# Optimization experiments

Hardware: AMD Instinct MI355X
Metric: run time of the kernel (lower is better)

Reference implementation:

```python
import jax, jax.numpy as jnp
import numpy as np

N_NODES = 100000
N_EDGES = 1600000
R = 8
EPS = 1e-5


def bn_eval(x, g, b, m, v):
    # BatchNorm1d in eval mode: affine with running stats
    return (x - m) * (g / jnp.sqrt(v + EPS)) + b


def rgcn_conv(x, W, root, bias, src, dst, etype):
    # PyG RGCNConv: out[i] = sum_r mean_{j in N_r(i)} x_j W_r + x_i W_root + b
    # Transform once per relation, then gather per edge (avoids [E,in,out] weight gather).
    h = jnp.einsum('ni,rio->rno', x, W)          # [R, N, O]
    msg = h[etype, src]                           # [E, O] gather
    key = dst * R + etype                         # per-(dst, relation) segment
    ones = jnp.ones(etype.shape, dtype=x.dtype)
    deg = jax.ops.segment_sum(ones, key, num_segments=N_NODES * R)
    norm = 1.0 / jnp.maximum(deg[key], 1.0)       # mean within each relation
    agg = jax.ops.segment_sum(msg * norm[:, None], dst, num_segments=N_NODES)
    return agg + x @ root + bias


def setup_inputs() -> dict:
    key = jax.random.key(0)
    ks = jax.random.split(key, 24)
    f = jnp.float32
    inp = {
        'n_id': jax.random.randint(ks[0], (N_NODES,), 0, N_NODES),
        'edge_index': jax.random.randint(ks[1], (2, N_EDGES), 0, N_NODES),
        'edge_types': jax.random.randint(ks[2], (N_EDGES,), 0, R),
        'emb': jax.random.normal(ks[3], (N_NODES, 32), f),
        'W1': jax.random.normal(ks[4], (R, 32, 64), f) * 0.1,
        'root1': jax.random.normal(ks[5], (32, 64), f) * 0.1,
        'b1': jax.random.normal(ks[6], (64,), f) * 0.1,
        'W2': jax.random.normal(ks[7], (R, 64, 64), f) * 0.1,
        'root2': jax.random.normal(ks[8], (64, 64), f) * 0.1,
        'b2': jax.random.normal(ks[9], (64,), f) * 0.1,
        'bn32_g': jax.random.uniform(ks[10], (32,), f, 0.5, 1.5),
        'bn32_b': jax.random.normal(ks[11], (32,), f) * 0.1,
        'bn32_m': jax.random.normal(ks[12], (32,), f) * 0.1,
        'bn32_v': jax.random.uniform(ks[13], (32,), f, 0.5, 1.5),
        'bn64_g': jax.random.uniform(ks[14], (64,), f, 0.5, 1.5),
        'bn64_b': jax.random.normal(ks[15], (64,), f) * 0.1,
        'bn64_m': jax.random.normal(ks[16], (64,), f) * 0.1,
        'bn64_v': jax.random.uniform(ks[17], (64,), f, 0.5, 1.5),
        'bn64b_g': jax.random.uniform(ks[18], (64,), f, 0.5, 1.5),
        'bn64b_b': jax.random.normal(ks[19], (64,), f) * 0.1,
        'bn64b_m': jax.random.normal(ks[20], (64,), f) * 0.1,
        'bn64b_v': jax.random.uniform(ks[21], (64,), f, 0.5, 1.5),
    }
    return inp


def reference(n_id, edge_index, edge_types, emb, W1, root1, b1, W2, root2, b2,
              bn32_g, bn32_b, bn32_m, bn32_v,
              bn64_g, bn64_b, bn64_m, bn64_v,
              bn64b_g, bn64b_b, bn64b_m, bn64b_v):
    src, dst = edge_index[0], edge_index[1]
    x = emb[n_id]                                  # embedding lookup
    x = bn_eval(x, bn32_g, bn32_b, bn32_m, bn32_v)
    x = jax.nn.relu(rgcn_conv(x, W1, root1, b1, src, dst, edge_types))
    x = bn_eval(x, bn64_g, bn64_b, bn64_m, bn64_v)
    # dropout is identity in eval mode
    x = rgcn_conv(x, W2, root2, b2, src, dst, edge_types)
    x = bn_eval(x, bn64b_g, bn64b_b, bn64b_m, bn64b_v)
    return x
```

## Files before the change

kernel.cpp:

```cpp
#include <hip/hip_runtime.h>

#define EPS 1e-5f
constexpr int NN  = 100000;
constexpr int NE  = 1600000;
constexpr int R   = 8;
constexpr int NBK = NN / 16;
constexpr int CAP = 512;
constexpr int CHUNK  = 2048;
constexpr int NCHUNK = (NE + CHUNK - 1) / CHUNK;
constexpr int NBIN   = 98;
constexpr int SEGS   = 9;
constexpr int BINCAP = SEGS * CHUNK;

typedef _Float16 half8 __attribute__((ext_vector_type(8)));
typedef _Float16 h2    __attribute__((ext_vector_type(2)));
typedef float f32x4 __attribute__((ext_vector_type(4)));

static __device__ inline unsigned short f2h(float f) {
    _Float16 h = (_Float16)f;
    return __builtin_bit_cast(unsigned short, h);
}

__global__ __launch_bounds__(256) void compute_x0(
    const int* __restrict__ n_id, const float* __restrict__ emb,
    const float* __restrict__ g, const float* __restrict__ b,
    const float* __restrict__ m, const float* __restrict__ v,
    unsigned int* __restrict__ x0)
{
    int idx = blockIdx.x * 256 + threadIdx.x;
    if (idx >= NN * 16) return;
    int i = idx >> 4, c = (idx & 15) * 2;
    int nid = n_id[i];
    float2 e = *reinterpret_cast<const float2*>(&emb[nid * 32 + c]);
    float s0 = g[c]     / sqrtf(v[c]     + EPS);
    float s1 = g[c + 1] / sqrtf(v[c + 1] + EPS);
    float y0 = (e.x - m[c])     * s0 + b[c];
    float y1 = (e.y - m[c + 1]) * s1 + b[c + 1];
    x0[idx] = (unsigned int)f2h(y0) | ((unsigned int)f2h(y1) << 16);
}

__global__ __launch_bounds__(256) void binner(
    const int* __restrict__ ei, const int* __restrict__ et,
    int* __restrict__ gcur, unsigned int* __restrict__ binreg)
{
    __shared__ unsigned pay[CHUNK];
    __shared__ unsigned short bof[CHUNK];
    __shared__ unsigned srt[CHUNK];
    __shared__ unsigned short sb[CHUNK];
    __shared__ int hist[NBIN], lstart[NBIN], lcur[NBIN], gbase[NBIN];
    __shared__ int scanbuf[NBIN];

    const int tid = threadIdx.x;
    const int base = blockIdx.x * CHUNK;
    const int n = min(CHUNK, NE - base);

    for (int t = tid; t < NBIN; t += 256) hist[t] = 0;
    __syncthreads();

    for (int t = tid; t < n; t += 256) {
        int e = base + t;
        int dst = ei[NE + e];
        int bin = dst >> 10;
        pay[t] = (unsigned)ei[e] | ((unsigned)et[e] << 17) |
                 ((unsigned)(dst & 1023) << 20);
        bof[t] = (unsigned short)bin;
        atomicAdd(&hist[bin], 1);
    }
    __syncthreads();

    if (tid < NBIN) scanbuf[tid] = hist[tid];
    __syncthreads();
    for (int d = 1; d < NBIN; d <<= 1) {
        int v = 0;
        if (tid < NBIN && tid >= d) v = scanbuf[tid - d];
        __syncthreads();
        if (tid < NBIN) scanbuf[tid] += v;
        __syncthreads();
    }
    if (tid < NBIN) {
        int h = hist[tid];
        int excl = scanbuf[tid] - h;
        lstart[tid] = excl;
        lcur[tid]   = excl;
        gbase[tid]  = (h > 0) ? atomicAdd(&gcur[tid], h) : 0;
    }
    __syncthreads();

    for (int t = tid; t < n; t += 256) {
        int b = bof[t];
        int s = atomicAdd(&lcur[b], 1);
        srt[s] = pay[t];
        sb[s]  = (unsigned short)b;
    }
    __syncthreads();

    for (int s = tid; s < n; s += 256) {
        int b = sb[s];
        int pos = gbase[b] + (s - lstart[b]);
        if (pos < BINCAP)
            binreg[(size_t)b * BINCAP + pos] = srt[s];
    }
}

__global__ __launch_bounds__(256) void refine(
    const unsigned int* __restrict__ binreg, const int* __restrict__ gcur,
    int* __restrict__ bcnt, unsigned int* __restrict__ sedge)
{
    __shared__ unsigned pay[CHUNK];
    __shared__ unsigned short bof[CHUNK];
    __shared__ unsigned srt[CHUNK];
    __shared__ unsigned short sb[CHUNK];
    __shared__ int hist[64], lstart[64], lcur[64], gbase[64];
    __shared__ int scanbuf[64];

    const int tid = threadIdx.x;
    const int bin = blockIdx.x / SEGS;
    const int seg = blockIdx.x % SEGS;
    const int nbin = min(gcur[bin], BINCAP);
    const int s0 = seg * CHUNK;
    if (s0 >= nbin) return;
    const int n = min(CHUNK, nbin - s0);

    for (int t = tid; t < 64; t += 256) hist[t] = 0;
    __syncthreads();

    for (int t = tid; t < n; t += 256) {
        unsigned p = binreg[(size_t)bin * BINCAP + s0 + t];
        int bb = (p >> 24) & 63;
        pay[t] = p;
        bof[t] = (unsigned short)bb;
        atomicAdd(&hist[bb], 1);
    }
    __syncthreads();

    if (tid < 64) scanbuf[tid] = hist[tid];
    __syncthreads();
    for (int d = 1; d < 64; d <<= 1) {
        int v = 0;
        if (tid < 64 && tid >= d) v = scanbuf[tid - d];
        __syncthreads();
        if (tid < 64) scanbuf[tid] += v;
        __syncthreads();
    }
    if (tid < 64) {
        int h = hist[tid];
        int excl = scanbuf[tid] - h;
        lstart[tid] = excl;
        lcur[tid]   = excl;
        int bucket = bin * 64 + tid;
        gbase[tid] = (h > 0 && bucket < NBK) ? atomicAdd(&bcnt[bucket], h) : 0;
    }
    __syncthreads();

    for (int t = tid; t < n; t += 256) {
        int b = bof[t];
        int s = atomicAdd(&lcur[b], 1);
        srt[s] = pay[t];
        sb[s]  = (unsigned short)b;
    }
    __syncthreads();

    for (int s = tid; s < n; s += 256) {
        int bb = sb[s];
        unsigned p = srt[s];
        unsigned src = p & 0x1FFFF;
        unsigned r   = (p >> 17) & 7;
        unsigned g   = (p >> 20) & 15;
        int bucket = bin * 64 + bb;
        int pos = gbase[bb] + (s - lstart[bb]);
        if (pos < CAP)
            sedge[(size_t)bucket * CAP + pos] = src | (r << 20) | (g << 23);
    }
}

template <int CIN>
__global__ __launch_bounds__(256) void pack_B(
    const float* __restrict__ Wrel,
    const float* __restrict__ Wroot,
    unsigned short* __restrict__ Bp)
{
    constexpr int K = 9 * CIN, KS = K / 32;
    int idx = blockIdx.x * 256 + threadIdx.x;
    if (idx >= 4 * KS * 64) return;
    int l = idx & 63;
    int rest = idx >> 6;
    int s = rest % KS;
    int t = rest / KS;
    int kb = s * 32 + (l >> 4) * 8;
    int col = t * 16 + (l & 15);
    unsigned short* dst = &Bp[(size_t)idx * 8];
#pragma unroll
    for (int j = 0; j < 8; ++j) {
        int k = kb + j;
        float w = (k < CIN) ? Wroot[k * 64 + col]
                            : Wrel[(size_t)(k - CIN) * 64 + col];
        dst[j] = f2h(w);
    }
}

__global__ __launch_bounds__(64) void prep_scales(
    const float* g1, const float* b1, const float* m1, const float* v1,
    float* sc1, float* sh1,
    const float* g2, const float* b2, const float* m2, const float* v2,
    float* sc2, float* sh2)
{
    int o = threadIdx.x;
    float s1 = g1[o] / sqrtf(v1[o] + EPS);
    sc1[o] = s1;
    sh1[o] = b1[o] - m1[o] * s1;
    float s2 = g2[o] / sqrtf(v2[o] + EPS);
    sc2[o] = s2;
    sh2[o] = b2[o] - m2[o] * s2;
}

template <int CIN, bool APPLY_RELU, bool OUT_F16>
__global__ __launch_bounds__(256) void fused_layer(
    const unsigned short* __restrict__ x,
    const unsigned int* __restrict__ sedge,
    const int* __restrict__ bcnt,
    const unsigned short* __restrict__ Bp,
    const float* __restrict__ bias,
    const float* __restrict__ scale, const float* __restrict__ shift,
    void* __restrict__ outv)
{
    constexpr int NB  = 16;
    constexpr int K   = 9 * CIN;
    constexpr int KS  = K / 32;
    constexpr int Kp  = K + 8;
    constexpr int VEC = CIN / 16;

    __shared__ unsigned short As[NB][Kp];
    __shared__ unsigned int   raw[CAP];
    __shared__ unsigned int   srt[CAP];
    __shared__ int cnt128[128];
    __shared__ int segoff[129];
    __shared__ int cur[128];

    const int node0 = blockIdx.x * NB;
    const int tid = threadIdx.x;
    const int nloc = min(bcnt[blockIdx.x], CAP);

    if (tid < 128) cnt128[tid] = 0;
    for (int t = tid; t < NB * (CIN / 4); t += 256) {
        int g = t / (CIN / 4), q = (t % (CIN / 4)) * 4;
        *reinterpret_cast<uint2*>(&As[g][q]) =
            *reinterpret_cast<const uint2*>(&x[(size_t)(node0 + g) * CIN + q]);
    }
    {
        uint4 z = {0u, 0u, 0u, 0u};
        for (int t = tid; t < NB * CIN; t += 256) {
            int g = t / CIN, q = (t % CIN) * 8;
            *reinterpret_cast<uint4*>(&As[g][CIN + q]) = z;
        }
    }
    __syncthreads();

    for (int t = tid; t < nloc; t += 256) {
        unsigned se = sedge[(size_t)blockIdx.x * CAP + t];
        raw[t] = se;
        atomicAdd(&cnt128[(se >> 20) & 127], 1);
    }
    __syncthreads();

    for (int d = 1; d < 128; d <<= 1) {
        int v = 0;
        if (tid < 128 && tid >= d) v = cnt128[tid - d];
        __syncthreads();
        if (tid < 128) cnt128[tid] += v;
        __syncthreads();
    }
    if (tid < 128) segoff[tid + 1] = cnt128[tid];
    if (tid == 0) segoff[0] = 0;
    __syncthreads();
    if (tid < 128) cur[tid] = segoff[tid];
    __syncthreads();

    for (int t = tid; t < nloc; t += 256) {
        unsigned se = raw[t];
        int k = (se >> 20) & 127;
        int slot = atomicAdd(&cur[k], 1);
        srt[slot] = se;
    }
    __syncthreads();

    {
        const int lx = tid & 15;
        const int g  = tid >> 4;
        const int c0 = lx * VEC;
        const int s = segoff[g * 8];
        const int e = segoff[g * 8 + 8];

        h2 a01 = {(_Float16)0, (_Float16)0};
        h2 a23 = {(_Float16)0, (_Float16)0};
        int cur_r = -1, cnt = 0;

        auto flushrun = [&]() {
            if (cnt > 0) {
                _Float16 ih = (_Float16)(1.0f / (float)cnt);
                h2 iv = {ih, ih};
                if constexpr (VEC == 4) {
                    uint2 pk;
                    pk.x = __builtin_bit_cast(unsigned, (h2)(a01 * iv));
                    pk.y = __builtin_bit_cast(unsigned, (h2)(a23 * iv));
                    *reinterpret_cast<uint2*>(&As[g][CIN + cur_r * CIN + c0]) = pk;
                    a23 = (h2){(_Float16)0, (_Float16)0};
                } else {
                    unsigned pk = __builtin_bit_cast(unsigned, (h2)(a01 * iv));
                    *reinterpret_cast<unsigned*>(&As[g][CIN + cur_r * CIN + c0]) = pk;
                }
                a01 = (h2){(_Float16)0, (_Float16)0};
            }
        };
        auto proc = [&](unsigned se, uint2 xv) {
            int r = (int)((se >> 20) & 7);
            if (r != cur_r) { flushrun(); cur_r = r; cnt = 0; }
            a01 += __builtin_bit_cast(h2, xv.x);
            if constexpr (VEC == 4)
                a23 += __builtin_bit_cast(h2, xv.y);
            ++cnt;
        };
        auto loadx = [&](unsigned se) -> uint2 {
            size_t base = (size_t)(se & 0xFFFFF) * CIN + c0;
            if constexpr (VEC == 4)
                return *reinterpret_cast<const uint2*>(&x[base]);
            else {
                uint2 r2; r2.x = *reinterpret_cast<const unsigned*>(&x[base]); r2.y = 0u;
                return r2;
            }
        };

        int j = s;
        for (; j + 4 <= e; j += 4) {
            unsigned se0 = srt[j],     se1 = srt[j + 1];
            unsigned se2 = srt[j + 2], se3 = srt[j + 3];
            uint2 x0v = loadx(se0);
            uint2 x1v = loadx(se1);
            uint2 x2v = loadx(se2);
            uint2 x3v = loadx(se3);
            proc(se0, x0v); proc(se1, x1v); proc(se2, x2v); proc(se3, x3v);
        }
        for (; j < e; ++j) {
            unsigned se0 = srt[j];
            proc(se0, loadx(se0));
        }
        flushrun();
    }
    __syncthreads();

    const int lane = tid & 63, wave = tid >> 6;
    const int arow = lane & 15;
    const int kb   = (lane >> 4) * 8;
    f32x4 acc = {0.f, 0.f, 0.f, 0.f};
    const unsigned short* a_ptr = &As[arow][kb];
    const unsigned short* b_ptr = &Bp[((size_t)(wave * KS) * 64 + lane) * 8];
#pragma unroll
    for (int ks = 0; ks < KS; ++ks) {
        half8 a = *reinterpret_cast<const half8*>(a_ptr + ks * 32);
        half8 b = *reinterpret_cast<const half8*>(b_ptr + (size_t)ks * 64 * 8);
        acc = __builtin_amdgcn_mfma_f32_16x16x32_f16(a, b, acc, 0, 0, 0);
    }

    const int o = wave * 16 + (lane & 15);
    const float sc = scale[o], sh = shift[o], bi = bias[o];
#pragma unroll
    for (int r = 0; r < 4; ++r) {
        int nrow = (lane >> 4) * 4 + r;
        float t = acc[r] + bi;
        if (APPLY_RELU) t = fmaxf(t, 0.0f);
        t = t * sc + sh;
        size_t oidx = (size_t)(node0 + nrow) * 64 + o;
        if (OUT_F16) ((unsigned short*)outv)[oidx] = f2h(t);
        else         ((float*)outv)[oidx] = t;
    }
}

extern "C" void kernel_launch(void* const* d_in, const int* in_sizes, int n_in,
                              void* d_out, int out_size, void* d_ws, size_t ws_size,
                              hipStream_t stream)
{
    const int*   n_id   = (const int*)d_in[0];
    const int*   ei     = (const int*)d_in[1];
    const int*   et     = (const int*)d_in[2];
    const float* emb    = (const float*)d_in[3];
    const float* W1     = (const float*)d_in[4];
    const float* root1  = (const float*)d_in[5];
    const float* b1     = (const float*)d_in[6];
    const float* W2     = (const float*)d_in[7];
    const float* root2  = (const float*)d_in[8];
    const float* b2     = (const float*)d_in[9];
    const float* bn32_g = (const float*)d_in[10];
    const float* bn32_b = (const float*)d_in[11];
    const float* bn32_m = (const float*)d_in[12];
    const float* bn32_v = (const float*)d_in[13];
    const float* bn64_g = (const float*)d_in[14];
    const float* bn64_b = (const float*)d_in[15];
    const float* bn64_m = (const float*)d_in[16];
    const float* bn64_v = (const float*)d_in[17];
    const float* bnb_g  = (const float*)d_in[18];
    const float* bnb_b  = (const float*)d_in[19];
    const float* bnb_m  = (const float*)d_in[20];
    const float* bnb_v  = (const float*)d_in[21];
    float* out = (float*)d_out;

    char* p = (char*)d_ws;
    int* gcur = (int*)p;                       p += (size_t)((NBIN + 3) & ~3) * 4;
    int* bcnt = (int*)p;                       p += (size_t)((NBK + 3) & ~3) * 4;
    unsigned int* binreg = (unsigned int*)p;   p += (size_t)NBIN * BINCAP * 4;
    unsigned int* sedge  = (unsigned int*)p;   p += (size_t)NBK * CAP * 4;
    unsigned short* x0  = (unsigned short*)p;  p += (size_t)NN * 32 * 2;
    unsigned short* h1  = (unsigned short*)p;  p += (size_t)NN * 64 * 2;
    unsigned short* Bp1 = (unsigned short*)p;  p += 4 * 9  * 64 * 8 * 2;
    unsigned short* Bp2 = (unsigned short*)p;  p += 4 * 18 * 64 * 8 * 2;
    float* sc1 = (float*)p;           p += 64 * 4;
    float* sh1 = (float*)p;           p += 64 * 4;
    float* sc2 = (float*)p;           p += 64 * 4;
    float* sh2 = (float*)p;           p += 64 * 4;

    hipMemsetAsync(gcur, 0, ((size_t)((NBIN + 3) & ~3) + (NBK + 3 & ~3)) * 4,
                   stream);
    binner<<<NCHUNK, 256, 0, stream>>>(ei, et, gcur, binreg);
    refine<<<NBIN * SEGS, 256, 0, stream>>>(binreg, gcur, bcnt, sedge);

    prep_scales<<<1, 64, 0, stream>>>(bn64_g, bn64_b, bn64_m, bn64_v, sc1, sh1,
                                      bnb_g, bnb_b, bnb_m, bnb_v, sc2, sh2);
    pack_B<32><<<(4 * 9 * 64 + 255) / 256, 256, 0, stream>>>(W1, root1, Bp1);
    pack_B<64><<<(4 * 18 * 64 + 255) / 256, 256, 0, stream>>>(W2, root2, Bp2);

    compute_x0<<<(NN * 16 + 255) / 256, 256, 0, stream>>>(
        n_id, emb, bn32_g, bn32_b, bn32_m, bn32_v, (unsigned int*)x0);
    fused_layer<32, true, true><<<NBK, 256, 0, stream>>>(
        x0, sedge, bcnt, Bp1, b1, sc1, sh1, h1);

    fused_layer<64, false, false><<<NBK, 256, 0, stream>>>(
        h1, sedge, bcnt, Bp2, b2, sc2, sh2, out);
}
```

Baseline: 158.3 us.

## Split each node's edge list across two 8-lane subgroups with wider loads

Each destination node's sorted edge range is now split at a relation boundary between two 8-thread subgroups instead of one 16-thread group. Each thread loads a wider vector per gathered row (16 bytes for CIN=64), so there are more independent gather streams per node. The raw shared staging buffer is also dropped, and edges are re-read from global memory for the scatter pass. The aim is more memory-level parallelism in the gather. The costs are a serial boundary search and imbalance when one relation run dominates.

```diff
diff --git a/kernel.cpp b/kernel.cpp
--- a/kernel.cpp
+++ b/kernel.cpp
@@ -227,10 +227,8 @@
     constexpr int K   = 9 * CIN;
     constexpr int KS  = K / 32;
     constexpr int Kp  = K + 8;
-    constexpr int VEC = CIN / 16;
 
     __shared__ unsigned short As[NB][Kp];
-    __shared__ unsigned int   raw[CAP];
     __shared__ unsigned int   srt[CAP];
     __shared__ int cnt128[128];
     __shared__ int segoff[129];
@@ -239,6 +237,7 @@
     const int node0 = blockIdx.x * NB;
     const int tid = threadIdx.x;
     const int nloc = min(bcnt[blockIdx.x], CAP);
+    const unsigned int* sedge_b = &sedge[(size_t)blockIdx.x * CAP];
 
     if (tid < 128) cnt128[tid] = 0;
     for (int t = tid; t < NB * (CIN / 4); t += 256) {
@@ -255,11 +254,8 @@
     }
     __syncthreads();
 
-    for (int t = tid; t < nloc; t += 256) {
-        unsigned se = sedge[(size_t)blockIdx.x * CAP + t];
-        raw[t] = se;
-        atomicAdd(&cnt128[(se >> 20) & 127], 1);
-    }
+    for (int t = tid; t < nloc; t += 256)
+        atomicAdd(&cnt128[(sedge_b[t] >> 20) & 127], 1);
     __syncthreads();
 
     for (int d = 1; d < 128; d <<= 1) {
@@ -276,7 +272,7 @@
     __syncthreads();
 
     for (int t = tid; t < nloc; t += 256) {
-        unsigned se = raw[t];
+        unsigned se = sedge_b[t];
         int k = (se >> 20) & 127;
         int slot = atomicAdd(&cur[k], 1);
         srt[slot] = se;
@@ -284,62 +280,85 @@
     __syncthreads();
 
     {
-        const int lx = tid & 15;
-        const int g  = tid >> 4;
-        const int c0 = lx * VEC;
+        const int sg   = tid >> 3;
+        const int ln   = tid & 7;
+        const int g    = sg >> 1;
+        const int half = sg & 1;
+        const int c0   = ln * (CIN / 8);
         const int s = segoff[g * 8];
         const int e = segoff[g * 8 + 8];
 
-        h2 a01 = {(_Float16)0, (_Float16)0};
-        h2 a23 = {(_Float16)0, (_Float16)0};
+        int mm = s + ((e - s + 1) >> 1);
+        if (mm > s && mm < e) {
+            int rprev = (srt[mm - 1] >> 20) & 7;
+            while (mm < e && (((srt[mm] >> 20) & 7) == rprev)) ++mm;
+        }
+        const int js = half ? mm : s;
+        const int je = half ? e  : mm;
+
+        h2 a0 = {(_Float16)0, (_Float16)0};
+        h2 a1 = {(_Float16)0, (_Float16)0};
+        h2 a2 = {(_Float16)0, (_Float16)0};
+        h2 a3 = {(_Float16)0, (_Float16)0};
         int cur_r = -1, cnt = 0;
 
         auto flushrun = [&]() {
             if (cnt > 0) {
                 _Float16 ih = (_Float16)(1.0f / (float)cnt);
                 h2 iv = {ih, ih};
-                if constexpr (VEC == 4) {
+                if constexpr (CIN == 64) {
+                    uint4 pk;
+                    pk.x = __builtin_bit_cast(unsigned, (h2)(a0 * iv));
+                    pk.y = __builtin_bit_cast(unsigned, (h2)(a1 * iv));
+                    pk.z = __builtin_bit_cast(unsigned, (h2)(a2 * iv));
+                    pk.w = __builtin_bit_cast(unsigned, (h2)(a3 * iv));
+                    *reinterpret_cast<uint4*>(&As[g][CIN + cur_r * CIN + c0]) = pk;
+                    a2 = (h2){(_Float16)0, (_Float16)0};
+                    a3 = (h2){(_Float16)0, (_Float16)0};
+                } else {
                     uint2 pk;
-                    pk.x = __builtin_bit_cast(unsigned, (h2)(a01 * iv));
-                    pk.y = __builtin_bit_cast(unsigned, (h2)(a23 * iv));
+                    pk.x = __builtin_bit_cast(unsigned, (h2)(a0 * iv));
+                    pk.y = __builtin_bit_cast(unsigned, (h2)(a1 * iv));
                     *reinterpret_cast<uint2*>(&As[g][CIN + cur_r * CIN + c0]) = pk;
-                    a23 = (h2){(_Float16)0, (_Float16)0};
-                } else {
-                    unsigned pk = __builtin_bit_cast(unsigned, (h2)(a01 * iv));
-                    *reinterpret_cast<unsigned*>(&As[g][CIN + cur_r * CIN + c0]) = pk;
+                    a1 = (h2){(_Float16)0, (_Float16)0};
                 }
-                a01 = (h2){(_Float16)0, (_Float16)0};
+                a0 = (h2){(_Float16)0, (_Float16)0};
+                if constexpr (CIN == 64)
+                    a1 = (h2){(_Float16)0, (_Float16)0};
             }
         };
-        auto proc = [&](unsigned se, uint2 xv) {
+        auto proc = [&](unsigned se, uint4 xv) {
             int r = (int)((se >> 20) & 7);
             if (r != cur_r) { flushrun(); cur_r = r; cnt = 0; }
-            a01 += __builtin_bit_cast(h2, xv.x);
-            if constexpr (VEC == 4)
-                a23 += __builtin_bit_cast(h2, xv.y);
+            a0 += __builtin_bit_cast(h2, xv.x);
+            a1 += __builtin_bit_cast(h2, xv.y);
+            if constexpr (CIN == 64) {
+                a2 += __builtin_bit_cast(h2, xv.z);
+                a3 += __builtin_bit_cast(h2, xv.w);
+            }
             ++cnt;
         };
-        auto loadx = [&](unsigned se) -> uint2 {
+        auto loadx = [&](unsigned se) -> uint4 {
             size_t base = (size_t)(se & 0xFFFFF) * CIN + c0;
-            if constexpr (VEC == 4)
-                return *reinterpret_cast<const uint2*>(&x[base]);
+            if constexpr (CIN == 64)
+                return *reinterpret_cast<const uint4*>(&x[base]);
             else {
-                uint2 r2; r2.x = *reinterpret_cast<const unsigned*>(&x[base]); r2.y = 0u;
-                return r2;
+                uint2 t2 = *reinterpret_cast<const uint2*>(&x[base]);
+                return make_uint4(t2.x, t2.y, 0u, 0u);
             }
         };
 
-        int j = s;
-        for (; j + 4 <= e; j += 4) {
+        int j = js;
+        for (; j + 4 <= je; j += 4) {
             unsigned se0 = srt[j],     se1 = srt[j + 1];
             unsigned se2 = srt[j + 2], se3 = srt[j + 3];
-            uint2 x0v = loadx(se0);
-            uint2 x1v = loadx(se1);
-            uint2 x2v = loadx(se2);
-            uint2 x3v = loadx(se3);
-            proc(se0, x0v); proc(se1, x1v); proc(se2, x2v); proc(se3, x3v);
+            uint4 v0 = loadx(se0);
+            uint4 v1 = loadx(se1);
+            uint4 v2 = loadx(se2);
+            uint4 v3 = loadx(se3);
+            proc(se0, v0); proc(se1, v1); proc(se2, v2); proc(se3, v3);
         }
-        for (; j < e; ++j) {
+        for (; j < je; ++j) {
             unsigned se0 = srt[j];
             proc(se0, loadx(se0));
         }
```

New measurement: 154.5 us. 1.02x faster.
